# Kernel optimization log

Measured on AMD Instinct MI355X. Metric: run time of the kernel, lower is better.

Reference implementation:

```python
import jax, jax.numpy as jnp
import numpy as np

N = 50000   # num nodes
E = 800000  # num edges (avg degree 16)
L = 4       # num_blocks
H = 128     # hidden_dim
CD = 3      # coords_dim
VD = 3      # vel_dim
FD = 16     # node feature dim = node_dim - coords_dim - vel_dim
ED = 16     # edge_dim
DIN = 2 * H + ED + 1  # edge MLP input dim = 273


def setup_inputs() -> dict:
    key = jax.random.key(0)
    ks = jax.random.split(key, 32)
    s = 0.05
    inp = {}
    inp['nodes'] = jax.random.normal(ks[0], (N, CD + VD + FD), jnp.float32)
    # avoid self-loops (start==end) so the coord-diff norm is never exactly 0
    start = jax.random.randint(ks[1], (E,), 0, N)
    off = jax.random.randint(ks[2], (E,), 1, N)
    inp['edge_indices'] = jnp.stack([start, (start + off) % N]).astype(jnp.int64)
    inp['edge_features'] = jax.random.normal(ks[3], (E, ED), jnp.float32)
    # node embedding
    inp['emb_w'] = (jax.random.normal(ks[4], (FD, H)) * s).astype(jnp.float32)
    inp['emb_b'] = jnp.zeros((H,), jnp.float32)
    # per-block params, stacked over L blocks
    def w(k, shape):
        return (jax.random.normal(k, shape) * s).astype(jnp.float32)
    inp['ew1'] = w(ks[5], (L, DIN, H)); inp['eb1'] = jnp.zeros((L, H), jnp.float32)
    inp['ew2'] = w(ks[6], (L, H, H));   inp['eb2'] = jnp.zeros((L, H), jnp.float32)
    inp['cw1'] = w(ks[7], (L, H, H));   inp['cb1'] = jnp.zeros((L, H), jnp.float32)
    inp['cw2'] = w(ks[8], (L, H, CD));  inp['cb2'] = jnp.zeros((L, CD), jnp.float32)
    inp['vw1'] = w(ks[9], (L, H, H));   inp['vb1'] = jnp.zeros((L, H), jnp.float32)
    inp['vw2'] = w(ks[10], (L, H, 1));  inp['vb2'] = jnp.zeros((L, 1), jnp.float32)
    inp['nw1'] = w(ks[11], (L, 2 * H, H)); inp['nb1'] = jnp.zeros((L, H), jnp.float32)
    inp['nw2'] = w(ks[12], (L, H, H));  inp['nb2'] = jnp.zeros((L, H), jnp.float32)
    return inp


def _forward(nodes, edge_features, emb_w, emb_b, ew1, eb1, ew2, eb2,
             cw1, cb1, cw2, cb2, vw1, vb1, vw2, vb2, nw1, nb1, nw2, nb2,
             edge_indices):
    silu = jax.nn.silu
    coords = nodes[:, :CD]
    vels = nodes[:, CD:CD + VD]
    h = nodes[:, CD + VD:] @ emb_w + emb_b  # [N, H]
    start, end = edge_indices[0], edge_indices[1]
    n = coords.shape[0]
    # per-node edge counts for the coordinate mean-aggregation
    cnt = jax.ops.segment_sum(jnp.ones((start.shape[0], 1), coords.dtype),
                              start, num_segments=n)
    cnt = jnp.maximum(cnt, 1.0)
    for l in range(L):
        cd = coords[start] - coords[end]                       # [E, CD]
        nrm = jnp.sqrt(jnp.sum(cd * cd, axis=1, keepdims=True))  # [E, 1]
        x = jnp.concatenate([h[start], h[end], nrm, edge_features], axis=1)
        m = silu(silu(x @ ew1[l] + eb1[l]) @ ew2[l] + eb2[l])  # [E, H]
        # coordinate update: mean-aggregated weighted diffs + velocity term
        ct = cd * (silu(m @ cw1[l] + cb1[l]) @ cw2[l] + cb2[l])
        coords = coords + jax.ops.segment_sum(ct, start, num_segments=n) / cnt
        coords = coords + (silu(h @ vw1[l] + vb1[l]) @ vw2[l] + vb2[l]) * vels
        # node update: sum-aggregated messages
        agg = jax.ops.segment_sum(m, start, num_segments=n)    # [N, H]
        h = h + silu(jnp.concatenate([h, agg], axis=1) @ nw1[l] + nb1[l]) @ nw2[l] + nb2[l]
    return coords  # prediction_type == 'coords'


def reference(nodes, edge_indices, edge_features, emb_w, emb_b,
              ew1, eb1, ew2, eb2, cw1, cb1, cw2, cb2,
              vw1, vb1, vw2, vb2, nw1, nb1, nw2, nb2):
    return _forward(nodes, edge_features, emb_w, emb_b, ew1, eb1, ew2, eb2,
                    cw1, cb1, cw2, cb2, vw1, vb1, vw2, vb2,
                    nw1, nb1, nw2, nb2, edge_indices)
```

## Files before the change

### kernel.cpp

```cpp
#include <hip/hip_runtime.h>

constexpr int NN = 50000;
constexpr int EE = 800000;
constexpr int HH = 128;

typedef __attribute__((ext_vector_type(8))) __bf16 bfv8;
typedef __attribute__((ext_vector_type(4))) float f32x4;
typedef __attribute__((ext_vector_type(16))) float f32x16;
typedef unsigned short u16;

__device__ __forceinline__ u16 f2bf(float x){
  unsigned u = __builtin_bit_cast(unsigned, x);
  u = u + 0x7fffu + ((u >> 16) & 1u);
  return (u16)(u >> 16);
}
__device__ __forceinline__ float fsilu(float x){
  return x * __builtin_amdgcn_rcpf(1.f + __expf(-x));
}

constexpr int SRB = 288;

template<int KS, int CBn>
__device__ __forceinline__ void mmW32(const u16* sB, const u16* __restrict__ Bp,
                                      const float* __restrict__ bias, int NB, f32x16* acc){
  const int lane = threadIdx.x & 63;
  const int col0 = lane & 31;
  #pragma unroll
  for (int cb = 0; cb < CBn; ++cb){
    int col = cb*32 + col0;
    float b = (col < NB) ? bias[col] : 0.f;
    #pragma unroll
    for (int r = 0; r < 16; ++r) acc[cb][r] = b;
  }
  const int row = lane & 31;
  const char* abase = (const char*)sB + row * SRB;
  const int kb = (lane >> 5) * 16;
  const int swz = (row & 15) << 4;
  const bfv8* __restrict__ bq = (const bfv8*)Bp + lane;
  #pragma unroll
  for (int ks = 0; ks < KS; ++ks){
    bfv8 a = *(const bfv8*)(abase + ((ks*32 + kb) ^ swz));
    #pragma unroll
    for (int cb = 0; cb < CBn; ++cb)
      acc[cb] = __builtin_amdgcn_mfma_f32_32x32x16_bf16(a, bq[(ks*CBn + cb) * 64], acc[cb], 0, 0, 0);
  }
}

template<int CBn>
__device__ __forceinline__ void silu_store32(const f32x16* acc, u16* sB){
  const int lane = threadIdx.x & 63;
  const int col0 = lane & 31;
  const int rbase = (lane >> 5) * 4;
  #pragma unroll
  for (int cb = 0; cb < CBn; ++cb){
    int col = cb*32 + col0;
    #pragma unroll
    for (int r = 0; r < 16; ++r){
      int row = (r & 3) + 8*(r >> 2) + rbase;
      *(u16*)((char*)sB + row*SRB + ((col*2) ^ ((row & 15) << 4))) = f2bf(fsilu(acc[cb][r]));
    }
  }
}

struct PackDesc { const float* src; u16* dst; int K; int Nc; int CB; int ksteps; int remap; int frag32; };
struct PackArgs { PackDesc d[32]; };

__global__ __launch_bounds__(256) void pack_kernel(PackArgs pa){
  PackDesc d = pa.d[blockIdx.x];
  int total = d.ksteps * d.CB * 512;
  for (int p = threadIdx.x; p < total; p += 256){
    int j = p & 7, lane = (p >> 3) & 63, unit = p >> 9;
    int cb = unit % d.CB, ks = unit / d.CB;
    int k, col;
    if (d.frag32){
      k = ks*16 + ((lane >> 5) * 8) + j;
      col = cb*32 + (lane & 31);
    } else {
      k = ks*32 + ((lane >> 4) * 8) + j;
      col = cb*16 + (lane & 15);
    }
    int kk = k;
    if (d.remap && k >= 256) kk = (k < 272) ? (k + 1) : ((k == 272) ? 256 : 0x7fffffff);
    float v = (kk < d.K && col < d.Nc) ? d.src[(size_t)kk * d.Nc + col] : 0.f;
    d.dst[p] = f2bf(v);
  }
}

__global__ __launch_bounds__(256) void embed_kernel(const float* __restrict__ nodes,
    const float* __restrict__ emb_w, const float* __restrict__ emb_b,
    float* __restrict__ hf, u16* __restrict__ hbf, float* __restrict__ coords){
  int t = blockIdx.x * 256 + threadIdx.x;
  int g = t >> 2, q = t & 3;
  if (g >= NN) return;
  const float* x = nodes + (size_t)g * 22;
  float acc[32];
  #pragma unroll
  for (int c = 0; c < 32; ++c) acc[c] = emb_b[q*32 + c];
  for (int k = 0; k < 16; ++k){
    float f = x[6 + k];
    const float* wr = emb_w + k*128 + q*32;
    #pragma unroll
    for (int c = 0; c < 32; ++c) acc[c] += f * wr[c];
  }
  size_t off = (size_t)g * HH + q*32;
  #pragma unroll
  for (int c = 0; c < 32; ++c){ hf[off + c] = acc[c]; hbf[off + c] = f2bf(acc[c]); }
  if (q == 0){
    coords[g*3+0] = x[0]; coords[g*3+1] = x[1]; coords[g*3+2] = x[2];
  }
}

__global__ __launch_bounds__(256) void count_kernel(const int* __restrict__ esrc, int* __restrict__ cnt_i){
  int e = blockIdx.x * 256 + threadIdx.x;
  if (e < EE) atomicAdd(&cnt_i[esrc[e]], 1);
}

__global__ __launch_bounds__(256) void scan_kernel(const int* __restrict__ cnt_i,
    int* __restrict__ row_start, int* __restrict__ fill){
  __shared__ int part[256];
  int t = threadIdx.x;
  int lo = t * 196, hi = lo + 196;
  if (lo > NN) lo = NN;
  if (hi > NN) hi = NN;
  int s = 0;
  for (int i = lo; i < hi; ++i) s += cnt_i[i];
  part[t] = s; __syncthreads();
  for (int d = 1; d < 256; d <<= 1){
    int v = (t >= d) ? part[t-d] : 0;
    __syncthreads();
    part[t] += v;
    __syncthreads();
  }
  int run = part[t] - s;
  for (int i = lo; i < hi; ++i){ row_start[i] = run; fill[i] = run; run += cnt_i[i]; }
  if (t == 255) row_start[NN] = run;
}

__global__ __launch_bounds__(256) void scatter_kernel(const int* __restrict__ esrc,
    const int* __restrict__ edst, int* __restrict__ fill,
    int2* __restrict__ sd_sorted, int* __restrict__ eid_sorted){
  int e = blockIdx.x * 256 + threadIdx.x;
  if (e < EE){
    int s = esrc[e];
    int pos = atomicAdd(&fill[s], 1);
    sd_sorted[pos] = make_int2(s, edst[e]);
    eid_sorted[pos] = e;
  }
}

__global__ __launch_bounds__(256) void edge_kernel(
    const float* __restrict__ coords, const u16* __restrict__ hbf, const float* __restrict__ ef,
    const int2* __restrict__ sd_sorted, const int* __restrict__ eid_sorted,
    const u16* __restrict__ ew1p, const u16* __restrict__ ew2p,
    const u16* __restrict__ cw1p, const u16* __restrict__ cw2p,
    const float* __restrict__ eb1, const float* __restrict__ eb2,
    const float* __restrict__ cb1, const float* __restrict__ cb2,
    float* __restrict__ agg, float* __restrict__ acc_ct){
  __shared__ __align__(16) u16 sBuf[4][32 * SRB / 2];
  __shared__ float4 s_cdn[128];
  __shared__ int s_src[132];
  __shared__ int s_eid[128];

  const int tid = threadIdx.x, wid = tid >> 6, lane = tid & 63;
  const int R = wid * 32;
  const int e0 = blockIdx.x * 128;

  if (lane < 32){
    int row = R + lane;
    int e = e0 + row;
    int2 sd = sd_sorted[e];
    float cx = coords[sd.x*3+0] - coords[sd.y*3+0];
    float cy = coords[sd.x*3+1] - coords[sd.y*3+1];
    float cz = coords[sd.x*3+2] - coords[sd.y*3+2];
    float nrm = sqrtf(cx*cx + cy*cy + cz*cz);
    s_cdn[row] = make_float4(cx, cy, cz, nrm);
    s_src[row] = sd.x; s_eid[row] = eid_sorted[e];
  }
  if (tid == 0) s_src[128] = -1;

  const int myrow = R + (lane & 31);
  const int kh = lane >> 5;
  int2 sd = sd_sorted[e0 + myrow];
  const u16* hsb = hbf + (size_t)sd.x * HH + kh*8;
  const u16* hdb = hbf + (size_t)sd.y * HH + kh*8;
  u16* sB = sBuf[wid];
  const int col0 = lane & 31;
  const int rbase4 = (lane >> 5) * 4;

  f32x16 acc[4];
  {
    const bfv8* __restrict__ bq = (const bfv8*)ew1p + lane;
    #pragma unroll
    for (int cb = 0; cb < 4; ++cb){
      float b = eb1[cb*32 + col0];
      #pragma unroll
      for (int r = 0; r < 16; ++r) acc[cb][r] = b;
    }
    #pragma unroll
    for (int ks = 0; ks < 8; ++ks){
      bfv8 a = *(const bfv8*)(hsb + ks*16);
      #pragma unroll
      for (int cb = 0; cb < 4; ++cb)
        acc[cb] = __builtin_amdgcn_mfma_f32_32x32x16_bf16(a, bq[(ks*4 + cb)*64], acc[cb], 0, 0, 0);
    }
    #pragma unroll
    for (int ks = 8; ks < 16; ++ks){
      bfv8 a = *(const bfv8*)(hdb + (ks - 8)*16);
      #pragma unroll
      for (int cb = 0; cb < 4; ++cb)
        acc[cb] = __builtin_amdgcn_mfma_f32_32x32x16_bf16(a, bq[(ks*4 + cb)*64], acc[cb], 0, 0, 0);
    }
    const int my_eid = s_eid[myrow];
    union { bfv8 v; u16 s[8]; unsigned u[4]; } a16, a17;
    {
      float4 f0 = *(const float4*)(ef + (size_t)my_eid * 16 + kh*8);
      float4 f1 = *(const float4*)(ef + (size_t)my_eid * 16 + kh*8 + 4);
      a16.u[0] = f2bf(f0.x) | ((unsigned)f2bf(f0.y) << 16);
      a16.u[1] = f2bf(f0.z) | ((unsigned)f2bf(f0.w) << 16);
      a16.u[2] = f2bf(f1.x) | ((unsigned)f2bf(f1.y) << 16);
      a16.u[3] = f2bf(f1.z) | ((unsigned)f2bf(f1.w) << 16);
    }
    a17.u[0] = a17.u[1] = a17.u[2] = a17.u[3] = 0u;
    if (kh == 0) a17.s[0] = f2bf(s_cdn[myrow].w);
    #pragma unroll
    for (int cb = 0; cb < 4; ++cb){
      acc[cb] = __builtin_amdgcn_mfma_f32_32x32x16_bf16(a16.v, bq[(16*4 + cb)*64], acc[cb], 0, 0, 0);
      acc[cb] = __builtin_amdgcn_mfma_f32_32x32x16_bf16(a17.v, bq[(17*4 + cb)*64], acc[cb], 0, 0, 0);
    }
  }
  silu_store32<4>(acc, sB);

  mmW32<8, 4>(sB, ew2p, eb2, 128, acc);
  {
    #pragma unroll
    for (int cb = 0; cb < 4; ++cb){
      int col = cb*32 + col0;
      #pragma unroll
      for (int grp = 0; grp < 4; ++grp){
        float run = 0.f;
        #pragma unroll
        for (int j = 0; j < 4; ++j){
          int r = grp*4 + j;
          int row = grp*8 + rbase4 + j;
          int grow = R + row;
          float m = fsilu(acc[cb][r]);
          run += m;
          *(u16*)((char*)sB + row*SRB + ((col*2) ^ ((row & 15) << 4))) = f2bf(m);
          int src = s_src[grow];
          if (j == 3 || s_src[grow + 1] != src){
            atomicAdd(&agg[(size_t)src * HH + col], run);
            run = 0.f;
          }
        }
      }
    }
  }

  mmW32<8, 4>(sB, cw1p, cb1, 128, acc);
  silu_store32<4>(acc, sB);

  f32x16 a4[1];
  mmW32<8, 1>(sB, cw2p, cb2, 3, a4);
  {
    if (col0 < 3){
      #pragma unroll
      for (int grp = 0; grp < 4; ++grp){
        float run = 0.f;
        #pragma unroll
        for (int j = 0; j < 4; ++j){
          int r = grp*4 + j;
          int row = grp*8 + rbase4 + j;
          int grow = R + row;
          float4 cdn = s_cdn[grow];
          float cdv = (col0 == 0) ? cdn.x : ((col0 == 1) ? cdn.y : cdn.z);
          run += cdv * a4[0][r];
          int src = s_src[grow];
          if (j == 3 || s_src[grow + 1] != src){
            atomicAdd(&acc_ct[(size_t)src * 3 + col0], run);
            run = 0.f;
          }
        }
      }
    }
  }
}

__device__ __forceinline__ void mm_lds1(const u16* Arows, const u16* __restrict__ Bp,
                                        const float* __restrict__ bias, int NB, int CBn,
                                        int KS, f32x4* acc){
  const int lane = threadIdx.x & 63;
  for (int cb = 0; cb < CBn; ++cb){
    int col = cb*16 + (lane & 15);
    float b = (col < NB) ? bias[col] : 0.f;
    acc[cb] = (f32x4){b, b, b, b};
  }
  const int arow = lane & 15;
  const char* abase = (const char*)Arows + arow * 256;
  const int kb = (lane >> 4) * 16;
  const int swz = (arow & 7) << 4;
  const bfv8* __restrict__ bq = (const bfv8*)Bp + lane;
  for (int ks = 0; ks < KS; ++ks){
    bfv8 a = *(const bfv8*)(abase + ((ks*64 + kb) ^ swz));
    for (int cb = 0; cb < CBn; ++cb)
      acc[cb] = __builtin_amdgcn_mfma_f32_16x16x32_bf16(a, bq[(ks*CBn + cb) * 64], acc[cb], 0, 0, 0);
  }
}

__global__ __launch_bounds__(256, 4) void node_kernel(
    float* __restrict__ coords, float* __restrict__ hf, u16* __restrict__ hbf,
    const float* __restrict__ agg, const float* __restrict__ acc_ct, const int* __restrict__ row_start,
    const float* __restrict__ nodes,
    const u16* __restrict__ vw1p, const u16* __restrict__ vw2p,
    const u16* __restrict__ nw1p, const u16* __restrict__ nw2p,
    const float* __restrict__ vb1, const float* __restrict__ vb2,
    const float* __restrict__ nb1, const float* __restrict__ nb2){
  __shared__ __align__(16) u16 sV[4][2048];
  __shared__ float s_vt[64];

  const int tid = threadIdx.x, wid = tid >> 6, lane = tid & 63;
  const int R = wid * 16;
  const int g0 = blockIdx.x * 64;

  const int myrow = R + (lane & 15);
  const int gnode = g0 + myrow;
  const int arow = (gnode < NN) ? gnode : (NN - 1);
  const int g = lane >> 4;
  const u16*  hb = hbf + (size_t)arow * HH + g*8;
  const float* ab = agg + (size_t)arow * HH + g*8;

  f32x4 acc[8];
  {
    const bfv8* __restrict__ bq = (const bfv8*)vw1p + lane;
    #pragma unroll
    for (int cb = 0; cb < 8; ++cb){
      float b = vb1[cb*16 + (lane & 15)];
      acc[cb] = (f32x4){b, b, b, b};
    }
    #pragma unroll
    for (int ks = 0; ks < 4; ++ks){
      bfv8 a = *(const bfv8*)(hb + ks*32);
      #pragma unroll
      for (int cb = 0; cb < 8; ++cb)
        acc[cb] = __builtin_amdgcn_mfma_f32_16x16x32_bf16(a, bq[(ks*8 + cb)*64], acc[cb], 0, 0, 0);
    }
  }
  {
    #pragma unroll
    for (int cb = 0; cb < 8; ++cb){
      #pragma unroll
      for (int j = 0; j < 4; ++j){
        int row = ((lane >> 4) << 2) + j;
        int col = cb*16 + (lane & 15);
        *(u16*)((char*)sV[wid] + row*256 + ((col*2) ^ ((row & 7) << 4))) = f2bf(fsilu(acc[cb][j]));
      }
    }
  }
  f32x4 a1[1];
  mm_lds1(sV[wid], vw2p, vb2, 1, 1, 4, a1);
  if ((lane & 15) == 0){
    #pragma unroll
    for (int j = 0; j < 4; ++j) s_vt[R + ((lane >> 4) << 2) + j] = a1[0][j];
  }
  if (lane < 16){
    int row = R + lane, gg = g0 + row;
    if (gg < NN){
      float cn = (float)(row_start[gg + 1] - row_start[gg]);
      if (cn < 1.f) cn = 1.f;
      float vt = s_vt[row];
      #pragma unroll
      for (int c = 0; c < 3; ++c){
        float val = coords[gg*3 + c] + acc_ct[gg*3 + c] / cn + vt * nodes[(size_t)gg*22 + 3 + c];
        coords[gg*3 + c] = val;
      }
    }
  }

  {
    const bfv8* __restrict__ bq = (const bfv8*)nw1p + lane;
    #pragma unroll
    for (int cb = 0; cb < 8; ++cb){
      float b = nb1[cb*16 + (lane & 15)];
      acc[cb] = (f32x4){b, b, b, b};
    }
    #pragma unroll
    for (int ks = 0; ks < 4; ++ks){
      bfv8 a = *(const bfv8*)(hb + ks*32);
      #pragma unroll
      for (int cb = 0; cb < 8; ++cb)
        acc[cb] = __builtin_amdgcn_mfma_f32_16x16x32_bf16(a, bq[(ks*8 + cb)*64], acc[cb], 0, 0, 0);
    }
    #pragma unroll
    for (int ks = 4; ks < 8; ++ks){
      float4 f0 = *(const float4*)(ab + (ks - 4)*32);
      float4 f1 = *(const float4*)(ab + (ks - 4)*32 + 4);
      union { bfv8 v; unsigned u[4]; } aa;
      aa.u[0] = f2bf(f0.x) | ((unsigned)f2bf(f0.y) << 16);
      aa.u[1] = f2bf(f0.z) | ((unsigned)f2bf(f0.w) << 16);
      aa.u[2] = f2bf(f1.x) | ((unsigned)f2bf(f1.y) << 16);
      aa.u[3] = f2bf(f1.z) | ((unsigned)f2bf(f1.w) << 16);
      #pragma unroll
      for (int cb = 0; cb < 8; ++cb)
        acc[cb] = __builtin_amdgcn_mfma_f32_16x16x32_bf16(aa.v, bq[(ks*8 + cb)*64], acc[cb], 0, 0, 0);
    }
  }
  {
    #pragma unroll
    for (int cb = 0; cb < 8; ++cb){
      #pragma unroll
      for (int j = 0; j < 4; ++j){
        int row = ((lane >> 4) << 2) + j;
        int col = cb*16 + (lane & 15);
        *(u16*)((char*)sV[wid] + row*256 + ((col*2) ^ ((row & 7) << 4))) = f2bf(fsilu(acc[cb][j]));
      }
    }
  }
  mm_lds1(sV[wid], nw2p, nb2, 128, 8, 4, acc);
  {
    #pragma unroll
    for (int cb = 0; cb < 8; ++cb){
      int col = cb*16 + (lane & 15);
      #pragma unroll
      for (int j = 0; j < 4; ++j){
        int row = R + ((lane >> 4) << 2) + j, gg = g0 + row;
        if (gg < NN){
          size_t off = (size_t)gg * HH + col;
          float h = acc[cb][j] + hf[off];
          hf[off] = h;
          hbf[off] = f2bf(h);
        }
      }
    }
  }
}

extern "C" void kernel_launch(void* const* d_in, const int* in_sizes, int n_in,
                              void* d_out, int out_size, void* d_ws, size_t ws_size,
                              hipStream_t stream){
  const float* nodes = (const float*)d_in[0];
  const int*   eidx  = (const int*)d_in[1];
  const float* ef    = (const float*)d_in[2];
  const float* emb_w = (const float*)d_in[3];
  const float* emb_b = (const float*)d_in[4];
  const float* ew1 = (const float*)d_in[5];
  const float* eb1 = (const float*)d_in[6];
  const float* ew2 = (const float*)d_in[7];
  const float* eb2 = (const float*)d_in[8];
  const float* cw1 = (const float*)d_in[9];
  const float* cb1 = (const float*)d_in[10];
  const float* cw2 = (const float*)d_in[11];
  const float* cb2 = (const float*)d_in[12];
  const float* vw1 = (const float*)d_in[13];
  const float* vb1 = (const float*)d_in[14];
  const float* vw2 = (const float*)d_in[15];
  const float* vb2 = (const float*)d_in[16];
  const float* nw1 = (const float*)d_in[17];
  const float* nb1 = (const float*)d_in[18];
  const float* nw2 = (const float*)d_in[19];
  const float* nb2 = (const float*)d_in[20];

  constexpr size_t WS_NEEDED = 78u * 1024u * 1024u;
  if (ws_size < WS_NEEDED) return;

  char* ws = (char*)d_ws;
  size_t off = 0;
  auto alloc = [&](size_t bytes){ void* p = ws + off; off += (bytes + 255) & ~(size_t)255; return p; };
  float* coords   = (float*)alloc((size_t)NN * 3 * 4);
  float* hf       = (float*)alloc((size_t)NN * HH * 4);
  u16*   hbf      = (u16*)  alloc((size_t)NN * HH * 2);
  float* agg      = (float*)alloc((size_t)NN * 131 * 4);
  float* acc_ct   = agg + (size_t)NN * HH;
  int*   cnt_i    = (int*)  alloc((size_t)NN * 4);
  int*   row_start= (int*)  alloc((size_t)(NN + 1) * 4);
  int*   fill     = (int*)  alloc((size_t)NN * 4);
  int2*  sd_sorted= (int2*) alloc((size_t)EE * 8);
  int*   eid_sorted=(int*)  alloc((size_t)EE * 4);

  constexpr int O_EW1 = 0;
  constexpr int O_EW2 = O_EW1 + 18*4*512;
  constexpr int O_CW1 = O_EW2 + 8*4*512;
  constexpr int O_CW2 = O_CW1 + 8*4*512;
  constexpr int O_VW1 = O_CW2 + 8*1*512;
  constexpr int O_VW2 = O_VW1 + 4*8*512;
  constexpr int O_NW1 = O_VW2 + 4*1*512;
  constexpr int O_NW2 = O_NW1 + 8*8*512;
  constexpr int LAYER_PACK = O_NW2 + 4*8*512;
  u16* packs = (u16*)alloc((size_t)LAYER_PACK * 4 * 2);

  PackArgs pa;
  for (int l = 0; l < 4; ++l){
    u16* base = packs + (size_t)l * LAYER_PACK;
    int i = l * 8;
    pa.d[i+0] = { ew1 + (size_t)l*273*128, base + O_EW1, 273, 128, 4, 18, 1, 1 };
    pa.d[i+1] = { ew2 + (size_t)l*128*128, base + O_EW2, 128, 128, 4,  8, 0, 1 };
    pa.d[i+2] = { cw1 + (size_t)l*128*128, base + O_CW1, 128, 128, 4,  8, 0, 1 };
    pa.d[i+3] = { cw2 + (size_t)l*128*3,   base + O_CW2, 128,   3, 1,  8, 0, 1 };
    pa.d[i+4] = { vw1 + (size_t)l*128*128, base + O_VW1, 128, 128, 8,  4, 0, 0 };
    pa.d[i+5] = { vw2 + (size_t)l*128*1,   base + O_VW2, 128,   1, 1,  4, 0, 0 };
    pa.d[i+6] = { nw1 + (size_t)l*256*128, base + O_NW1, 256, 128, 8,  8, 0, 0 };
    pa.d[i+7] = { nw2 + (size_t)l*128*128, base + O_NW2, 128, 128, 8,  4, 0, 0 };
  }

  pack_kernel<<<32, 256, 0, stream>>>(pa);
  embed_kernel<<<(NN*4 + 255)/256, 256, 0, stream>>>(nodes, emb_w, emb_b, hf, hbf, coords);
  hipMemsetAsync(cnt_i, 0, (size_t)NN * 4, stream);
  count_kernel<<<(EE + 255)/256, 256, 0, stream>>>(eidx, cnt_i);
  scan_kernel<<<1, 256, 0, stream>>>(cnt_i, row_start, fill);
  scatter_kernel<<<(EE + 255)/256, 256, 0, stream>>>(eidx, eidx + EE, fill, sd_sorted, eid_sorted);

  for (int l = 0; l < 4; ++l){
    hipMemsetAsync(agg, 0, (size_t)NN * 131 * 4, stream);
    u16* base = packs + (size_t)l * LAYER_PACK;
    edge_kernel<<<EE/128, 256, 0, stream>>>(coords, hbf, ef, sd_sorted, eid_sorted,
        base + O_EW1, base + O_EW2, base + O_CW1, base + O_CW2,
        eb1 + l*128, eb2 + l*128, cb1 + l*128, cb2 + l*3, agg, acc_ct);
    node_kernel<<<(NN + 63)/64, 256, 0, stream>>>(coords, hf, hbf, agg, acc_ct, row_start, nodes,
        base + O_VW1, base + O_VW2, base + O_NW1, base + O_NW2,
        vb1 + l*128, vb2 + l, nb1 + l*128, nb2 + l*128);
  }

  hipMemcpyAsync(d_out, coords, (size_t)NN * 3 * 4, hipMemcpyDeviceToDevice, stream);
}
```

Measured before the change: 2.060 ms.

## Process two 32-edge tiles per wave to reuse weight fragments across MFMAs

Each wave of the edge kernel now handles 64 edges as two 32-row tiles. Every weight fragment loaded from global memory feeds two MFMAs, one per tile, which halves weight-load traffic per edge and exposes more independent MFMA chains. The block covers 256 edges, so the grid is halved, and LDS use doubles to eight tile buffers. Accumulator registers double (two sets of 4 f32x16), which may lower occupancy or cause spills.

```diff
diff --git a/kernel.cpp b/kernel.cpp
--- a/kernel.cpp
+++ b/kernel.cpp
@@ -21,8 +21,9 @@
 constexpr int SRB = 288;
 
 template<int KS, int CBn>
-__device__ __forceinline__ void mmW32(const u16* sB, const u16* __restrict__ Bp,
-                                      const float* __restrict__ bias, int NB, f32x16* acc){
+__device__ __forceinline__ void mmW32_2(const u16* sA, const u16* sBt, const u16* __restrict__ Bp,
+                                        const float* __restrict__ bias, int NB,
+                                        f32x16* accA, f32x16* accB){
   const int lane = threadIdx.x & 63;
   const int col0 = lane & 31;
   #pragma unroll
@@ -30,19 +31,25 @@
     int col = cb*32 + col0;
     float b = (col < NB) ? bias[col] : 0.f;
     #pragma unroll
-    for (int r = 0; r < 16; ++r) acc[cb][r] = b;
+    for (int r = 0; r < 16; ++r){ accA[cb][r] = b; accB[cb][r] = b; }
   }
   const int row = lane & 31;
-  const char* abase = (const char*)sB + row * SRB;
   const int kb = (lane >> 5) * 16;
   const int swz = (row & 15) << 4;
+  const char* aA = (const char*)sA + row * SRB;
+  const char* aB = (const char*)sBt + row * SRB;
   const bfv8* __restrict__ bq = (const bfv8*)Bp + lane;
   #pragma unroll
   for (int ks = 0; ks < KS; ++ks){
-    bfv8 a = *(const bfv8*)(abase + ((ks*32 + kb) ^ swz));
-    #pragma unroll
-    for (int cb = 0; cb < CBn; ++cb)
-      acc[cb] = __builtin_amdgcn_mfma_f32_32x32x16_bf16(a, bq[(ks*CBn + cb) * 64], acc[cb], 0, 0, 0);
+    int off = (ks*32 + kb) ^ swz;
+    bfv8 vA = *(const bfv8*)(aA + off);
+    bfv8 vB = *(const bfv8*)(aB + off);
+    #pragma unroll
+    for (int cb = 0; cb < CBn; ++cb){
+      bfv8 b = bq[(ks*CBn + cb) * 64];
+      accA[cb] = __builtin_amdgcn_mfma_f32_32x32x16_bf16(vA, b, accA[cb], 0, 0, 0);
+      accB[cb] = __builtin_amdgcn_mfma_f32_32x32x16_bf16(vB, b, accB[cb], 0, 0, 0);
+    }
   }
 }
 
@@ -156,16 +163,16 @@
     const float* __restrict__ eb1, const float* __restrict__ eb2,
     const float* __restrict__ cb1, const float* __restrict__ cb2,
     float* __restrict__ agg, float* __restrict__ acc_ct){
-  __shared__ __align__(16) u16 sBuf[4][32 * SRB / 2];
-  __shared__ float4 s_cdn[128];
-  __shared__ int s_src[132];
-  __shared__ int s_eid[128];
+  __shared__ __align__(16) u16 sBuf[8][32 * SRB / 2];
+  __shared__ float4 s_cdn[256];
+  __shared__ int s_src[260];
+  __shared__ int s_eid[256];
 
   const int tid = threadIdx.x, wid = tid >> 6, lane = tid & 63;
-  const int R = wid * 32;
-  const int e0 = blockIdx.x * 128;
-
-  if (lane < 32){
+  const int R = wid * 64;
+  const int e0 = blockIdx.x * 256;
+
+  {
     int row = R + lane;
     int e = e0 + row;
     int2 sd = sd_sorted[e];
@@ -176,108 +183,152 @@
     s_cdn[row] = make_float4(cx, cy, cz, nrm);
     s_src[row] = sd.x; s_eid[row] = eid_sorted[e];
   }
-  if (tid == 0) s_src[128] = -1;
-
-  const int myrow = R + (lane & 31);
+  if (tid == 0) s_src[256] = -1;
+
+  const int er = lane & 31;
   const int kh = lane >> 5;
-  int2 sd = sd_sorted[e0 + myrow];
-  const u16* hsb = hbf + (size_t)sd.x * HH + kh*8;
-  const u16* hdb = hbf + (size_t)sd.y * HH + kh*8;
-  u16* sB = sBuf[wid];
+  const int rA = R + er, rB = R + 32 + er;
+  int2 sdA = sd_sorted[e0 + rA];
+  int2 sdB = sd_sorted[e0 + rB];
+  const u16* hsA = hbf + (size_t)sdA.x * HH + kh*8;
+  const u16* hdA = hbf + (size_t)sdA.y * HH + kh*8;
+  const u16* hsB = hbf + (size_t)sdB.x * HH + kh*8;
+  const u16* hdB = hbf + (size_t)sdB.y * HH + kh*8;
+  u16* scA = sBuf[wid];
+  u16* scB = sBuf[wid + 4];
   const int col0 = lane & 31;
-  const int rbase4 = (lane >> 5) * 4;
-
-  f32x16 acc[4];
+  const int rbase4 = kh * 4;
+
+  f32x16 accA[4], accB[4];
   {
     const bfv8* __restrict__ bq = (const bfv8*)ew1p + lane;
     #pragma unroll
     for (int cb = 0; cb < 4; ++cb){
       float b = eb1[cb*32 + col0];
       #pragma unroll
-      for (int r = 0; r < 16; ++r) acc[cb][r] = b;
+      for (int r = 0; r < 16; ++r){ accA[cb][r] = b; accB[cb][r] = b; }
     }
     #pragma unroll
     for (int ks = 0; ks < 8; ++ks){
-      bfv8 a = *(const bfv8*)(hsb + ks*16);
-      #pragma unroll
-      for (int cb = 0; cb < 4; ++cb)
-        acc[cb] = __builtin_amdgcn_mfma_f32_32x32x16_bf16(a, bq[(ks*4 + cb)*64], acc[cb], 0, 0, 0);
+      bfv8 vA = *(const bfv8*)(hsA + ks*16);
+      bfv8 vB = *(const bfv8*)(hsB + ks*16);
+      #pragma unroll
+      for (int cb = 0; cb < 4; ++cb){
+        bfv8 b = bq[(ks*4 + cb)*64];
+        accA[cb] = __builtin_amdgcn_mfma_f32_32x32x16_bf16(vA, b, accA[cb], 0, 0, 0);
+        accB[cb] = __builtin_amdgcn_mfma_f32_32x32x16_bf16(vB, b, accB[cb], 0, 0, 0);
+      }
     }
     #pragma unroll
     for (int ks = 8; ks < 16; ++ks){
-      bfv8 a = *(const bfv8*)(hdb + (ks - 8)*16);
-      #pragma unroll
-      for (int cb = 0; cb < 4; ++cb)
-        acc[cb] = __builtin_amdgcn_mfma_f32_32x32x16_bf16(a, bq[(ks*4 + cb)*64], acc[cb], 0, 0, 0);
-    }
-    const int my_eid = s_eid[myrow];
-    union { bfv8 v; u16 s[8]; unsigned u[4]; } a16, a17;
+      bfv8 vA = *(const bfv8*)(hdA + (ks - 8)*16);
+      bfv8 vB = *(const bfv8*)(hdB + (ks - 8)*16);
+      #pragma unroll
+      for (int cb = 0; cb < 4; ++cb){
+        bfv8 b = bq[(ks*4 + cb)*64];
+        accA[cb] = __builtin_amdgcn_mfma_f32_32x32x16_bf16(vA, b, accA[cb], 0, 0, 0);
+        accB[cb] = __builtin_amdgcn_mfma_f32_32x32x16_bf16(vB, b, accB[cb], 0, 0, 0);
+      }
+    }
+    union U { bfv8 v; u16 s[8]; unsigned u[4]; };
+    U a16A, a16B, a17A, a17B;
     {
-      float4 f0 = *(const float4*)(ef + (size_t)my_eid * 16 + kh*8);
-      float4 f1 = *(const float4*)(ef + (size_t)my_eid * 16 + kh*8 + 4);
-      a16.u[0] = f2bf(f0.x) | ((unsigned)f2bf(f0.y) << 16);
-      a16.u[1] = f2bf(f0.z) | ((unsigned)f2bf(f0.w) << 16);
-      a16.u[2] = f2bf(f1.x) | ((unsigned)f2bf(f1.y) << 16);
-      a16.u[3] = f2bf(f1.z) | ((unsigned)f2bf(f1.w) << 16);
-    }
-    a17.u[0] = a17.u[1] = a17.u[2] = a17.u[3] = 0u;
-    if (kh == 0) a17.s[0] = f2bf(s_cdn[myrow].w);
+      const float* efA = ef + (size_t)s_eid[rA] * 16 + kh*8;
+      float4 f0 = *(const float4*)efA;
+      float4 f1 = *(const float4*)(efA + 4);
+      a16A.u[0] = f2bf(f0.x) | ((unsigned)f2bf(f0.y) << 16);
+      a16A.u[1] = f2bf(f0.z) | ((unsigned)f2bf(f0.w) << 16);
+      a16A.u[2] = f2bf(f1.x) | ((unsigned)f2bf(f1.y) << 16);
+      a16A.u[3] = f2bf(f1.z) | ((unsigned)f2bf(f1.w) << 16);
+      const float* efB = ef + (size_t)s_eid[rB] * 16 + kh*8;
+      float4 g0 = *(const float4*)efB;
+      float4 g1 = *(const float4*)(efB + 4);
+      a16B.u[0] = f2bf(g0.x) | ((unsigned)f2bf(g0.y) << 16);
+      a16B.u[1] = f2bf(g0.z) | ((unsigned)f2bf(g0.w) << 16);
+      a16B.u[2] = f2bf(g1.x) | ((unsigned)f2bf(g1.y) << 16);
+      a16B.u[3] = f2bf(g1.z) | ((unsigned)f2bf(g1.w) << 16);
+    }
+    a17A.u[0]=a17A.u[1]=a17A.u[2]=a17A.u[3]=0u;
+    a17B.u[0]=a17B.u[1]=a17B.u[2]=a17B.u[3]=0u;
+    if (kh == 0){
+      a17A.s[0] = f2bf(s_cdn[rA].w);
+      a17B.s[0] = f2bf(s_cdn[rB].w);
+    }
     #pragma unroll
     for (int cb = 0; cb < 4; ++cb){
-      acc[cb] = __builtin_amdgcn_mfma_f32_32x32x16_bf16(a16.v, bq[(16*4 + cb)*64], acc[cb], 0, 0, 0);
-      acc[cb] = __builtin_amdgcn_mfma_f32_32x32x16_bf16(a17.v, bq[(17*4 + cb)*64], acc[cb], 0, 0, 0);
-    }
-  }
-  silu_store32<4>(acc, sB);
-
-  mmW32<8, 4>(sB, ew2p, eb2, 128, acc);
+      bfv8 b16 = bq[(16*4 + cb)*64];
+      bfv8 b17 = bq[(17*4 + cb)*64];
+      accA[cb] = __builtin_amdgcn_mfma_f32_32x32x16_bf16(a16A.v, b16, accA[cb], 0, 0, 0);
+      accB[cb] = __builtin_amdgcn_mfma_f32_32x32x16_bf16(a16B.v, b16, accB[cb], 0, 0, 0);
+      accA[cb] = __builtin_amdgcn_mfma_f32_32x32x16_bf16(a17A.v, b17, accA[cb], 0, 0, 0);
+      accB[cb] = __builtin_amdgcn_mfma_f32_32x32x16_bf16(a17B.v, b17, accB[cb], 0, 0, 0);
+    }
+  }
+  silu_store32<4>(accA, scA);
+  silu_store32<4>(accB, scB);
+
+  mmW32_2<8, 4>(scA, scB, ew2p, eb2, 128, accA, accB);
   {
     #pragma unroll
     for (int cb = 0; cb < 4; ++cb){
       int col = cb*32 + col0;
       #pragma unroll
       for (int grp = 0; grp < 4; ++grp){
-        float run = 0.f;
+        float runA = 0.f, runB = 0.f;
         #pragma unroll
         for (int j = 0; j < 4; ++j){
           int r = grp*4 + j;
           int row = grp*8 + rbase4 + j;
-          int grow = R + row;
-          float m = fsilu(acc[cb][r]);
-          run += m;
-          *(u16*)((char*)sB + row*SRB + ((col*2) ^ ((row & 15) << 4))) = f2bf(m);
-          int src = s_src[grow];
-          if (j == 3 || s_src[grow + 1] != src){
-            atomicAdd(&agg[(size_t)src * HH + col], run);
-            run = 0.f;
+          float mA = fsilu(accA[cb][r]);
+          float mB = fsilu(accB[cb][r]);
+          runA += mA; runB += mB;
+          int sw = (col*2) ^ ((row & 15) << 4);
+          *(u16*)((char*)scA + row*SRB + sw) = f2bf(mA);
+          *(u16*)((char*)scB + row*SRB + sw) = f2bf(mB);
+          int gA = R + row, gB = R + 32 + row;
+          int srcA = s_src[gA], srcB = s_src[gB];
+          if (j == 3 || s_src[gA + 1] != srcA){
+            atomicAdd(&agg[(size_t)srcA * HH + col], runA);
+            runA = 0.f;
+          }
+          if (j == 3 || s_src[gB + 1] != srcB){
+            atomicAdd(&agg[(size_t)srcB * HH + col], runB);
+            runB = 0.f;
           }
         }
       }
     }
   }
 
-  mmW32<8, 4>(sB, cw1p, cb1, 128, acc);
-  silu_store32<4>(acc, sB);
-
-  f32x16 a4[1];
-  mmW32<8, 1>(sB, cw2p, cb2, 3, a4);
+  mmW32_2<8, 4>(scA, scB, cw1p, cb1, 128, accA, accB);
+  silu_store32<4>(accA, scA);
+  silu_store32<4>(accB, scB);
+
+  f32x16 a4A[1], a4B[1];
+  mmW32_2<8, 1>(scA, scB, cw2p, cb2, 3, a4A, a4B);
   {
     if (col0 < 3){
       #pragma unroll
       for (int grp = 0; grp < 4; ++grp){
-        float run = 0.f;
+        float runA = 0.f, runB = 0.f;
         #pragma unroll
         for (int j = 0; j < 4; ++j){
           int r = grp*4 + j;
           int row = grp*8 + rbase4 + j;
-          int grow = R + row;
-          float4 cdn = s_cdn[grow];
-          float cdv = (col0 == 0) ? cdn.x : ((col0 == 1) ? cdn.y : cdn.z);
-          run += cdv * a4[0][r];
-          int src = s_src[grow];
-          if (j == 3 || s_src[grow + 1] != src){
-            atomicAdd(&acc_ct[(size_t)src * 3 + col0], run);
-            run = 0.f;
+          int gA = R + row, gB = R + 32 + row;
+          float4 cA = s_cdn[gA], cB = s_cdn[gB];
+          float dA = (col0 == 0) ? cA.x : ((col0 == 1) ? cA.y : cA.z);
+          float dB = (col0 == 0) ? cB.x : ((col0 == 1) ? cB.y : cB.z);
+          runA += dA * a4A[0][r];
+          runB += dB * a4B[0][r];
+          int srcA = s_src[gA], srcB = s_src[gB];
+          if (j == 3 || s_src[gA + 1] != srcA){
+            atomicAdd(&acc_ct[(size_t)srcA * 3 + col0], runA);
+            runA = 0.f;
+          }
+          if (j == 3 || s_src[gB + 1] != srcB){
+            atomicAdd(&acc_ct[(size_t)srcB * 3 + col0], runB);
+            runB = 0.f;
           }
         }
       }
@@ -510,7 +561,7 @@
   for (int l = 0; l < 4; ++l){
     hipMemsetAsync(agg, 0, (size_t)NN * 131 * 4, stream);
     u16* base = packs + (size_t)l * LAYER_PACK;
-    edge_kernel<<<EE/128, 256, 0, stream>>>(coords, hbf, ef, sd_sorted, eid_sorted,
+    edge_kernel<<<EE/256, 256, 0, stream>>>(coords, hbf, ef, sd_sorted, eid_sorted,
         base + O_EW1, base + O_EW2, base + O_CW1, base + O_CW2,
         eb1 + l*128, eb2 + l*128, cb1 + l*128, cb2 + l*3, agg, acc_ct);
     node_kernel<<<(NN + 63)/64, 256, 0, stream>>>(coords, hf, hbf, agg, acc_ct, row_start, nodes,
```

Result: slower. 2.673 ms (+29.8%).
